# Performance work log

Measured on AMD Instinct MI355X. Metric: run time of the kernel, lower is better.

Reference implementation:

```python
import jax, jax.numpy as jnp
import numpy as np

B, F, C, T, K, P = 16, 32, 32, 2048, 129, 64  # P = conv padding; K-1-P = 64 -> same-length output


def setup_inputs() -> dict:
    key = jax.random.key(0)
    k0, k1, k2, k3, k4, k5 = jax.random.split(key, 6)
    coeffs = jax.random.normal(k0, (B, 2, F, 7, 5, T), dtype=jnp.float32)
    rows = jax.random.randint(k1, (C,), 0, 7, dtype=jnp.int32)
    cols = jax.random.randint(k2, (C,), 0, 5, dtype=jnp.int32)
    ri_scale = jax.random.uniform(k3, (F,), jnp.float32, 0.5, 1.5)
    ri_shift = jax.random.normal(k4, (F,), dtype=jnp.float32) * 0.1
    freq_gain = jnp.ones((F,), dtype=jnp.float32)
    # torch ConvTranspose1d weight: (in_channels=C*2F, out_channels/groups=1, K)
    synth_weight = jax.random.normal(k5, (C * 2 * F, 1, K), dtype=jnp.float32) / np.sqrt(2.0 * F * K)
    return {"coeffs": coeffs, "rows": rows, "cols": cols, "ri_scale": ri_scale,
            "ri_shift": ri_shift, "freq_gain": freq_gain, "synth_weight": synth_weight}


def reference(coeffs, rows, cols, ri_scale, ri_shift, freq_gain, synth_weight):
    Bc, _, Fq, _, _, Tt = coeffs.shape
    Cc = rows.shape[0]
    # fancy-index gather over the (7,5) electrode grid -> (B, 2, F, C, T)
    feat = coeffs[:, :, :, rows, cols, :]
    # normalize (ri stats broadcast over freq dim) then per-frequency gain
    fdim = (None, None, slice(None), None, None)
    feat = feat / (ri_scale[fdim] + 1e-12) - ri_shift[fdim]
    feat = feat * freq_gain[fdim]
    # permute (B,2,F,C,T) -> (B,C,2,F,T) and flatten to (B, C*2F, T)
    z = jnp.transpose(feat, (0, 3, 1, 2, 4)).reshape(Bc, Cc * 2 * Fq, Tt)
    # depthwise-grouped ConvTranspose1d (stride=1, padding=P) == grouped
    # cross-correlation with time-flipped kernel and padding K-1-P.
    Kk = synth_weight.shape[-1]
    w = synth_weight.reshape(Cc, 2 * Fq, Kk)[:, :, ::-1]  # (Cout=C, Cin/groups=2F, K)
    pad = Kk - 1 - P
    x_hat = jax.lax.conv_general_dilated(
        z, w, window_strides=(1,), padding=[(pad, pad)],
        feature_group_count=Cc, dimension_numbers=("NCH", "OIH", "NCH"))
    return x_hat  # (B, C, T)
```

## Files before the change

kernel.cpp:

```cpp
#include <hip/hip_runtime.h>

typedef __attribute__((ext_vector_type(8))) short short8;
typedef __attribute__((ext_vector_type(4))) float f32x4;

#define C_ 32
#define T_ 2048
#define K_ 129

__device__ __forceinline__ unsigned int bfround(float f) {
    unsigned int u = __float_as_uint(f);
    return u + 0x7fffu + ((u >> 16) & 1u);
}

__global__ __launch_bounds__(256) void wtoep_pack(
    const float* __restrict__ sw, unsigned short* __restrict__ wt)
{
    const int c = blockIdx.x, dd = blockIdx.y;
    const int t = threadIdx.x, l = t & 63, fw = t >> 6;
    const int m = l & 15, qb = (l >> 4) & 1, i2 = (l >> 5) & 1;
    const int d = dd - 4;
    for (int fr = fw; fr < 32; fr += 4) {
        const int iq = fr >> 2, igl = fr & 3;
        const int i = iq * 8 + igl * 2 + i2;
        unsigned short v[8];
        #pragma unroll
        for (int e = 0; e < 8; ++e) {
            const int tl = 8 * qb + e;
            const int j = 16 * d + 64 + m - tl;
            const float wv = (j >= 0 && j <= 128) ? sw[(c * 64 + i) * K_ + j] : 0.f;
            v[e] = (unsigned short)(bfround(wv) >> 16);
        }
        *(short8*)(wt + (((c * 9 + dd) * 32 + fr) * 64 + l) * 8) = *(short8*)v;
    }
}

__global__ __launch_bounds__(256, 3) void wavelet_synth_v5(
    const float* __restrict__ coeffs, const int* __restrict__ rows,
    const int* __restrict__ cols, const float* __restrict__ ri_scale,
    const float* __restrict__ ri_shift, const float* __restrict__ freq_gain,
    const unsigned short* __restrict__ wt, float* __restrict__ out)
{
    __shared__ __align__(16) unsigned char smem[49152];
    unsigned short* zs = (unsigned short*)smem;

    const int t  = threadIdx.x;
    const int g0 = blockIdx.x * 4;
    const int c  = blockIdx.y;
    const int rc = rows[c];
    const int cc = cols[c];

    const int lane = t & 63;
    const int w    = t >> 6;
    const int i2   = (lane >> 5) & 1;
    const int qb   = (lane >> 4) & 1;

    const int s_r  = t & 1;
    const int s_b  = (t >> 1) & 15;
    const int s_il = (t >> 5) & 7;

    f32x4 acc[12];
    #pragma unroll
    for (int a = 0; a < 12; ++a) acc[a] = (f32x4){0.f, 0.f, 0.f, 0.f};

    for (int iq = 0; iq < 8; ++iq) {
        const int i  = iq * 8 + s_il;
        const int f  = i & 31;
        const int ri = i >> 5;
        const float inv = __builtin_amdgcn_rcpf(ri_scale[f] + 1e-12f);
        const float Aa  = inv * freq_gain[f];
        const float Bb  = -ri_shift[f] * freq_gain[f];
        const long  row = ((long)(s_b * 2 + ri) * 32 + f) * 35 + rc * 5 + cc;
        const float* srcb = coeffs + row * T_ + g0 * 16 + s_r * 8;

        __syncthreads();
        #pragma unroll
        for (int vi = 0; vi < 4; ++vi) {
            const float4 x = *(const float4*)(srcb + vi * 16);
            const float4 y = *(const float4*)(srcb + vi * 16 + 4);
            float vv[8];
            vv[0] = x.x * Aa + Bb; vv[1] = x.y * Aa + Bb;
            vv[2] = x.z * Aa + Bb; vv[3] = x.w * Aa + Bb;
            vv[4] = y.x * Aa + Bb; vv[5] = y.y * Aa + Bb;
            vv[6] = y.z * Aa + Bb; vv[7] = y.w * Aa + Bb;
            unsigned short pk[8];
            #pragma unroll
            for (int e = 0; e < 8; ++e) pk[e] = (unsigned short)(bfround(vv[e]) >> 16);
            *(short8*)(zs + ((vi * 8 + s_il) * 16 + s_b) * 24 + s_r * 8) = *(short8*)pk;
        }
        __syncthreads();

        const unsigned short* wbase = wt + ((c * 9) * 32 + iq * 4 + w) * 512 + lane * 8;
        const unsigned short* zb =
            zs + ((w * 2 + i2) * 16 + (lane & 15)) * 24 + qb * 8;
        #pragma unroll
        for (int d = 0; d < 9; ++d) {
            const short8 afrag = *(const short8*)(wbase + d * 32 * 512);
            #pragma unroll
            for (int vi = 0; vi < 4; ++vi) {
                const short8 bf = *(const short8*)(zb + vi * (8 * 16 * 24));
                acc[vi + d] = __builtin_amdgcn_mfma_f32_16x16x32_bf16(
                    afrag, bf, acc[vi + d], 0, 0, 0);
            }
        }
    }

    __syncthreads();
    float* red = (float*)smem;
    #pragma unroll
    for (int a = 0; a < 12; ++a)
        *(f32x4*)(red + ((w * 12 + a) * 64 + lane) * 4) = acc[a];
    __syncthreads();

    {
        const int rb  = t >> 4;
        const int tau = t & 15;
        const int s   = tau >> 2;
        const int rr  = tau & 3;
        float* obase = out + ((long)rb * C_ + c) * T_ + tau;
        #pragma unroll
        for (int a = 0; a < 12; ++a) {
            const int o = g0 - 4 + a;
            if (o < 0 || o >= 128) continue;
            float sum = 0.f;
            #pragma unroll
            for (int ww = 0; ww < 4; ++ww)
                sum += red[((ww * 12 + a) * 64 + s * 16 + rb) * 4 + rr];
            unsafeAtomicAdd(obase + o * 16, sum);
        }
    }
}

extern "C" void kernel_launch(void* const* d_in, const int* in_sizes, int n_in,
                              void* d_out, int out_size, void* d_ws, size_t ws_size,
                              hipStream_t stream) {
    const float* coeffs    = (const float*)d_in[0];
    const int*   rows      = (const int*)d_in[1];
    const int*   cols      = (const int*)d_in[2];
    const float* ri_scale  = (const float*)d_in[3];
    const float* ri_shift  = (const float*)d_in[4];
    const float* freq_gain = (const float*)d_in[5];
    const float* sw        = (const float*)d_in[6];
    float* out = (float*)d_out;
    unsigned short* wt = (unsigned short*)d_ws;

    hipMemsetAsync(d_out, 0, (size_t)out_size, stream);
    hipLaunchKernelGGL(wtoep_pack, dim3(32, 9), dim3(256), 0, stream, sw, wt);
    hipLaunchKernelGGL(wavelet_synth_v5, dim3(32, 32), dim3(256), 0, stream,
                       coeffs, rows, cols, ri_scale, ri_shift, freq_gain, wt, out);
}
```

Baseline: 412.5 us.

## Double the time tile per block and prefetch next coeff chunk into registers

```diff
diff --git a/kernel.cpp b/kernel.cpp
--- a/kernel.cpp
+++ b/kernel.cpp
@@ -11,6 +11,13 @@
     unsigned int u = __float_as_uint(f);
     return u + 0x7fffu + ((u >> 16) & 1u);
 }
+
+#define BARRIER_LDS() do {                                   \
+    __builtin_amdgcn_sched_barrier(0);                       \
+    asm volatile("s_waitcnt lgkmcnt(0)" ::: "memory");       \
+    __builtin_amdgcn_s_barrier();                            \
+    __builtin_amdgcn_sched_barrier(0);                       \
+} while (0)
 
 __global__ __launch_bounds__(256) void wtoep_pack(
     const float* __restrict__ sw, unsigned short* __restrict__ wt)
@@ -34,17 +41,17 @@
     }
 }
 
-__global__ __launch_bounds__(256, 3) void wavelet_synth_v5(
+__global__ __launch_bounds__(256, 2) void wavelet_synth_v6(
     const float* __restrict__ coeffs, const int* __restrict__ rows,
     const int* __restrict__ cols, const float* __restrict__ ri_scale,
     const float* __restrict__ ri_shift, const float* __restrict__ freq_gain,
     const unsigned short* __restrict__ wt, float* __restrict__ out)
 {
-    __shared__ __align__(16) unsigned char smem[49152];
+    __shared__ __align__(16) unsigned char smem[65536];
     unsigned short* zs = (unsigned short*)smem;
 
     const int t  = threadIdx.x;
-    const int g0 = blockIdx.x * 4;
+    const int g0 = blockIdx.x * 8;
     const int c  = blockIdx.y;
     const int rc = rows[c];
     const int cc = cols[c];
@@ -58,25 +65,37 @@
     const int s_b  = (t >> 1) & 15;
     const int s_il = (t >> 5) & 7;
 
-    f32x4 acc[12];
+    f32x4 acc[16];
     #pragma unroll
-    for (int a = 0; a < 12; ++a) acc[a] = (f32x4){0.f, 0.f, 0.f, 0.f};
+    for (int a = 0; a < 16; ++a) acc[a] = (f32x4){0.f, 0.f, 0.f, 0.f};
+
+    float4 pf[16];
+    {
+        const int i  = s_il;
+        const int f  = i & 31;
+        const int ri = i >> 5;
+        const long row = ((long)(s_b * 2 + ri) * 32 + f) * 35 + rc * 5 + cc;
+        const float* src = coeffs + row * T_ + g0 * 16 + s_r * 8;
+        #pragma unroll
+        for (int vi = 0; vi < 8; ++vi) {
+            pf[vi * 2 + 0] = *(const float4*)(src + vi * 16);
+            pf[vi * 2 + 1] = *(const float4*)(src + vi * 16 + 4);
+        }
+    }
 
     for (int iq = 0; iq < 8; ++iq) {
-        const int i  = iq * 8 + s_il;
-        const int f  = i & 31;
-        const int ri = i >> 5;
+        const int i = iq * 8 + s_il;
+        const int f = i & 31;
         const float inv = __builtin_amdgcn_rcpf(ri_scale[f] + 1e-12f);
         const float Aa  = inv * freq_gain[f];
         const float Bb  = -ri_shift[f] * freq_gain[f];
-        const long  row = ((long)(s_b * 2 + ri) * 32 + f) * 35 + rc * 5 + cc;
-        const float* srcb = coeffs + row * T_ + g0 * 16 + s_r * 8;
 
-        __syncthreads();
+        BARRIER_LDS();
+
         #pragma unroll
-        for (int vi = 0; vi < 4; ++vi) {
-            const float4 x = *(const float4*)(srcb + vi * 16);
-            const float4 y = *(const float4*)(srcb + vi * 16 + 4);
+        for (int vi = 0; vi < 8; ++vi) {
+            const float4 x = pf[vi * 2 + 0];
+            const float4 y = pf[vi * 2 + 1];
             float vv[8];
             vv[0] = x.x * Aa + Bb; vv[1] = x.y * Aa + Bb;
             vv[2] = x.z * Aa + Bb; vv[3] = x.w * Aa + Bb;
@@ -87,29 +106,46 @@
             for (int e = 0; e < 8; ++e) pk[e] = (unsigned short)(bfround(vv[e]) >> 16);
             *(short8*)(zs + ((vi * 8 + s_il) * 16 + s_b) * 24 + s_r * 8) = *(short8*)pk;
         }
-        __syncthreads();
+
+        if (iq < 7) {
+            const int i1  = (iq + 1) * 8 + s_il;
+            const int f1  = i1 & 31;
+            const int ri1 = i1 >> 5;
+            const long row1 = ((long)(s_b * 2 + ri1) * 32 + f1) * 35 + rc * 5 + cc;
+            const float* src1 = coeffs + row1 * T_ + g0 * 16 + s_r * 8;
+            #pragma unroll
+            for (int vi = 0; vi < 8; ++vi) {
+                pf[vi * 2 + 0] = *(const float4*)(src1 + vi * 16);
+                pf[vi * 2 + 1] = *(const float4*)(src1 + vi * 16 + 4);
+            }
+        }
+
+        BARRIER_LDS();
 
         const unsigned short* wbase = wt + ((c * 9) * 32 + iq * 4 + w) * 512 + lane * 8;
         const unsigned short* zb =
             zs + ((w * 2 + i2) * 16 + (lane & 15)) * 24 + qb * 8;
+        short8 bfr[8];
+        #pragma unroll
+        for (int vi = 0; vi < 8; ++vi)
+            bfr[vi] = *(const short8*)(zb + vi * (8 * 16 * 24));
         #pragma unroll
         for (int d = 0; d < 9; ++d) {
             const short8 afrag = *(const short8*)(wbase + d * 32 * 512);
             #pragma unroll
-            for (int vi = 0; vi < 4; ++vi) {
-                const short8 bf = *(const short8*)(zb + vi * (8 * 16 * 24));
+            for (int vi = 0; vi < 8; ++vi) {
                 acc[vi + d] = __builtin_amdgcn_mfma_f32_16x16x32_bf16(
-                    afrag, bf, acc[vi + d], 0, 0, 0);
+                    afrag, bfr[vi], acc[vi + d], 0, 0, 0);
             }
         }
     }
 
-    __syncthreads();
+    BARRIER_LDS();
     float* red = (float*)smem;
     #pragma unroll
-    for (int a = 0; a < 12; ++a)
-        *(f32x4*)(red + ((w * 12 + a) * 64 + lane) * 4) = acc[a];
-    __syncthreads();
+    for (int a = 0; a < 16; ++a)
+        *(f32x4*)(red + ((w * 16 + a) * 64 + lane) * 4) = acc[a];
+    BARRIER_LDS();
 
     {
         const int rb  = t >> 4;
@@ -118,13 +154,13 @@
         const int rr  = tau & 3;
         float* obase = out + ((long)rb * C_ + c) * T_ + tau;
         #pragma unroll
-        for (int a = 0; a < 12; ++a) {
+        for (int a = 0; a < 16; ++a) {
             const int o = g0 - 4 + a;
             if (o < 0 || o >= 128) continue;
             float sum = 0.f;
             #pragma unroll
             for (int ww = 0; ww < 4; ++ww)
-                sum += red[((ww * 12 + a) * 64 + s * 16 + rb) * 4 + rr];
+                sum += red[((ww * 16 + a) * 64 + s * 16 + rb) * 4 + rr];
             unsafeAtomicAdd(obase + o * 16, sum);
         }
     }
@@ -145,6 +181,6 @@
 
     hipMemsetAsync(d_out, 0, (size_t)out_size, stream);
     hipLaunchKernelGGL(wtoep_pack, dim3(32, 9), dim3(256), 0, stream, sw, wt);
-    hipLaunchKernelGGL(wavelet_synth_v5, dim3(32, 32), dim3(256), 0, stream,
+    hipLaunchKernelGGL(wavelet_synth_v6, dim3(16, 32), dim3(256), 0, stream,
                        coeffs, rows, cols, ri_scale, ri_shift, freq_gain, wt, out);
 }
```

Result: faster. 398.2 us (-3.5%).
